# Kernel tuning notes

Measured on AMD Instinct MI355X. Metric: run time of the kernel, lower is better.

Reference implementation:

```python
import jax, jax.numpy as jnp
import numpy as np

N = 50000
E = 800000
IN_C, HID_C, OUT_C = 128, 128, 64


def _glorot(key, shape, gain=1.0):
    fan_in, fan_out = shape[0], shape[1]
    lim = gain * np.sqrt(6.0 / (fan_in + fan_out))
    return jax.random.uniform(key, shape, jnp.float32, -lim, lim)


def setup_inputs() -> dict:
    key = jax.random.key(0)
    ks = jax.random.split(key, 16)
    relu_gain = float(np.sqrt(2.0))
    x = jax.random.normal(ks[0], (N, IN_C), jnp.float32)
    src = jax.random.randint(ks[1], (E,), 0, N, jnp.int64)
    dst = jax.random.randint(ks[2], (E,), 0, N, jnp.int64)
    # layer 0: NGNN_GCNConv(IN_C -> HID_C -> HID_C)
    W0 = _glorot(ks[3], (IN_C, HID_C))
    b0 = jnp.zeros((HID_C,), jnp.float32)
    fcW = _glorot(ks[4], (HID_C, HID_C), relu_gain)
    fcb = jax.random.uniform(ks[5], (HID_C,), jnp.float32, -1, 1) / np.sqrt(HID_C)
    fc2W = _glorot(ks[6], (HID_C, HID_C), relu_gain)
    fc2b = jax.random.uniform(ks[7], (HID_C,), jnp.float32, -1, 1) / np.sqrt(HID_C)
    # layer 1: GraphConv(HID_C -> HID_C)
    W1 = _glorot(ks[8], (HID_C, HID_C))
    b1 = jnp.zeros((HID_C,), jnp.float32)
    # layer 2: GraphConv(HID_C -> OUT_C)
    W2 = _glorot(ks[9], (HID_C, OUT_C))
    b2 = jnp.zeros((OUT_C,), jnp.float32)
    return dict(x=x, src=src, dst=dst, W0=W0, b0=b0, fcW=fcW, fcb=fcb,
                fc2W=fc2W, fc2b=fc2b, W1=W1, b1=b1, W2=W2, b2=b2)


def _degree_norms(src, dst):
    ones = jnp.ones((E,), jnp.float32)
    deg_out = jnp.clip(jax.ops.segment_sum(ones, src, num_segments=N), 1.0)
    deg_in = jnp.clip(jax.ops.segment_sum(ones, dst, num_segments=N), 1.0)
    return jax.lax.rsqrt(deg_out), jax.lax.rsqrt(deg_in)


def _graph_conv(x, W, b, src, dst, nsrc, ndst):
    # DGL GraphConv, norm='both': out = D_in^{-1/2} A (D_out^{-1/2} x W) + b
    h = (x * nsrc[:, None]) @ W            # [N, out_c]
    agg = jax.ops.segment_sum(h[src], dst, num_segments=N)  # gather + scatter-add
    return agg * ndst[:, None] + b


def reference(x, src, dst, W0, b0, fcW, fcb, fc2W, fc2b, W1, b1, W2, b2):
    nsrc, ndst = _degree_norms(src, dst)
    # layer 0: NGNN_GCNConv -> relu (dropout: eval-mode identity)
    h = _graph_conv(x, W0, b0, src, dst, nsrc, ndst)
    h = jax.nn.relu(h)
    h = jax.nn.relu(h @ fcW + fcb)
    h = h @ fc2W + fc2b
    h = jax.nn.relu(h)
    # layer 1: GraphConv -> relu
    h = jax.nn.relu(_graph_conv(h, W1, b1, src, dst, nsrc, ndst))
    # layer 2: GraphConv (no activation)
    return _graph_conv(h, W2, b2, src, dst, nsrc, ndst)
```

## Files before the change

### kernel.cpp

```cpp
#include <hip/hip_runtime.h>
#include <hip/hip_bf16.h>

#define NN 50000
#define NE 800000
#define PAD 56

typedef __attribute__((ext_vector_type(8))) short bf16x8;
typedef __attribute__((ext_vector_type(4))) float f32x4;
typedef __attribute__((ext_vector_type(8))) unsigned short u16x8;

__device__ __forceinline__ unsigned short f2bf(float f) {
    __hip_bfloat16 h = __float2bfloat16(f);
    return *(unsigned short*)&h;
}
__device__ __forceinline__ float bf2f(unsigned short u) {
    unsigned int w = ((unsigned int)u) << 16;
    return __uint_as_float(w);
}

__device__ __forceinline__ void split8(const float* __restrict__ p, bf16x8& h8, bf16x8& l8) {
    float4 v0 = *(const float4*)p;
    float4 v1 = *(const float4*)(p + 4);
    float f[8] = {v0.x, v0.y, v0.z, v0.w, v1.x, v1.y, v1.z, v1.w};
#pragma unroll
    for (int i = 0; i < 8; ++i) {
        unsigned short h = f2bf(f[i]);
        h8[i] = (short)h;
        l8[i] = (short)f2bf(f[i] - bf2f(h));
    }
}

#define DEG_BLK 64
#define DEG_CHUNK 12500
#define DEG_WORDS 12500
#define GEMM0_BLK 782
#define CVW_ELEMS 57344
#define CVW_BLK 224

__global__ __launch_bounds__(256) void hists_kernel(
    const int* __restrict__ src, const int* __restrict__ dst,
    unsigned* __restrict__ psrc, unsigned* __restrict__ pdst,
    const float* __restrict__ x, const float* __restrict__ W0, unsigned short* __restrict__ Hb,
    const float* __restrict__ fcW, const float* __restrict__ fc2W,
    const float* __restrict__ W1, const float* __restrict__ W2,
    unsigned short* __restrict__ wp_hi, unsigned short* __restrict__ wp_lo) {
    __shared__ unsigned hist[DEG_WORDS];
    const int bid = blockIdx.x;
    const int tid = threadIdx.x;
    if (bid < 2 * DEG_BLK) {
        const int dblk = (bid < DEG_BLK) ? bid : bid - DEG_BLK;
        const int* ep = (bid < DEG_BLK) ? src : dst;
        unsigned* outp = ((bid < DEG_BLK) ? psrc : pdst) + (size_t)dblk * DEG_WORDS;
        for (int i = tid; i < DEG_WORDS; i += 256) hist[i] = 0;
        __syncthreads();
        const int4* sp = (const int4*)(ep + dblk * DEG_CHUNK);
        for (int i = tid; i < DEG_CHUNK / 4; i += 256) {
            int4 s = sp[i];
            atomicAdd(&hist[s.x >> 2], 1u << ((s.x & 3) * 8));
            atomicAdd(&hist[s.y >> 2], 1u << ((s.y & 3) * 8));
            atomicAdd(&hist[s.z >> 2], 1u << ((s.z & 3) * 8));
            atomicAdd(&hist[s.w >> 2], 1u << ((s.w & 3) * 8));
        }
        __syncthreads();
        for (int i = tid; i < DEG_WORDS; i += 256) outp[i] = hist[i];
    } else if (bid < 2 * DEG_BLK + CVW_BLK) {
        int t = (bid - 2 * DEG_BLK) * 256 + tid;
        if (t < CVW_ELEMS) {
            int mi = (t < 16384) ? 0 : (t < 32768) ? 1 : (t < 49152) ? 2 : 3;
            int beg = mi * 16384;
            int Cm = (mi == 3) ? 64 : 128;
            int loc = t - beg;
            int k = loc / Cm, c = loc % Cm;
            float v;
            switch (mi) {
                case 0: v = fcW[loc]; break;
                case 1: v = fc2W[loc]; break;
                case 2: v = W1[loc]; break;
                default: v = W2[loc]; break;
            }
            unsigned short h = f2bf(v);
            unsigned short l = f2bf(v - bf2f(h));
            int off = (((c >> 4) * 4 + (k >> 5)) * 64 + ((k & 31) >> 3) * 16 + (c & 15)) * 8 + (k & 7);
            wp_hi[beg + off] = h;
            wp_lo[beg + off] = l;
        }
    } else {
        const int gb = bid - 2 * DEG_BLK - CVW_BLK;
        const int wave = tid >> 6;
        const int lane = tid & 63;
        const int m = lane & 15, kg = lane >> 4;
        const int r0 = gb * 64 + wave * 16;
        int ar = r0 + m;
        ar = (ar < NN) ? ar : (NN - 1);

        bf16x8 ah[4], al[4];
#pragma unroll
        for (int ks = 0; ks < 4; ++ks)
            split8(&x[(size_t)ar * 128 + ks * 32 + kg * 8], ah[ks], al[ks]);

#pragma unroll
        for (int ct = 0; ct < 8; ++ct) {
            f32x4 acc = {0.f, 0.f, 0.f, 0.f};
            const int n = ct * 16 + m;
#pragma unroll
            for (int ks = 0; ks < 4; ++ks) {
                float w[8];
#pragma unroll
                for (int i = 0; i < 8; ++i)
                    w[i] = W0[(size_t)(ks * 32 + kg * 8 + i) * 128 + n];
                bf16x8 bh, bl;
#pragma unroll
                for (int i = 0; i < 8; ++i) {
                    unsigned short h = f2bf(w[i]);
                    bh[i] = (short)h;
                    bl[i] = (short)f2bf(w[i] - bf2f(h));
                }
                acc = __builtin_amdgcn_mfma_f32_16x16x32_bf16(ah[ks], bh, acc, 0, 0, 0);
                acc = __builtin_amdgcn_mfma_f32_16x16x32_bf16(al[ks], bh, acc, 0, 0, 0);
                acc = __builtin_amdgcn_mfma_f32_16x16x32_bf16(ah[ks], bl, acc, 0, 0, 0);
            }
#pragma unroll
            for (int j = 0; j < 4; ++j) {
                const int ra = r0 + 4 * kg + j;
                if (ra < NN) Hb[(size_t)ra * 128 + n] = f2bf(acc[j]);
            }
        }
    }
}

__global__ __launch_bounds__(256) void merge_scan(unsigned* __restrict__ psrc,
                                                  unsigned* __restrict__ pdst,
                                                  int* __restrict__ degout,
                                                  int* __restrict__ cnt) {
    const int idx = blockIdx.x * 256 + threadIdx.x;
    if (idx >= DEG_WORDS) return;
    {
        int a0 = 0, a1 = 0, a2 = 0, a3 = 0;
#pragma unroll 8
        for (int p = 0; p < DEG_BLK; ++p) {
            unsigned w = psrc[(size_t)p * DEG_WORDS + idx];
            a0 += w & 0xFF; a1 += (w >> 8) & 0xFF; a2 += (w >> 16) & 0xFF; a3 += (w >> 24);
        }
        ((int4*)degout)[idx] = make_int4(a0, a1, a2, a3);
    }
    {
        int r0 = 0, r1 = 0, r2 = 0, r3 = 0;
#pragma unroll 8
        for (int p = 0; p < DEG_BLK; ++p) {
            const size_t o = (size_t)p * DEG_WORDS + idx;
            unsigned w = pdst[o];
            pdst[o] = (unsigned)r0 | ((unsigned)r1 << 8) | ((unsigned)r2 << 16) | ((unsigned)r3 << 24);
            r0 += w & 0xFF; r1 += (w >> 8) & 0xFF; r2 += (w >> 16) & 0xFF; r3 += (w >> 24);
        }
        ((int4*)cnt)[idx] = make_int4(r0, r1, r2, r3);
    }
}

__global__ __launch_bounds__(256) void fillc_kernel(const int* __restrict__ src,
                                                    const int* __restrict__ dst,
                                                    const unsigned* __restrict__ pdst,
                                                    unsigned short* __restrict__ col) {
    __shared__ unsigned hist[DEG_WORDS];
    const int dblk = blockIdx.x;
    const int tid = threadIdx.x;
    const unsigned* bp = pdst + (size_t)dblk * DEG_WORDS;
    for (int i = tid; i < DEG_WORDS; i += 256) hist[i] = bp[i];
    __syncthreads();
    const int4* sp = (const int4*)(src + dblk * DEG_CHUNK);
    const int4* dp = (const int4*)(dst + dblk * DEG_CHUNK);
    for (int i = tid; i < DEG_CHUNK / 4; i += 256) {
        int4 s = sp[i];
        int4 d = dp[i];
#pragma unroll
        for (int u = 0; u < 4; ++u) {
            const int dd = (u == 0) ? d.x : (u == 1) ? d.y : (u == 2) ? d.z : d.w;
            const int ss = (u == 0) ? s.x : (u == 1) ? s.y : (u == 2) ? s.z : s.w;
            const unsigned sh = (dd & 3) * 8;
            const unsigned old = atomicAdd(&hist[dd >> 2], 1u << sh);
            const int slot = (old >> sh) & 0xFF;
            col[dd * PAD + slot] = (unsigned short)ss;
        }
    }
}

template <int C>
__global__ __launch_bounds__(256) void mfma_gemm(
    const float* __restrict__ A,
    const unsigned short* __restrict__ Bhi, const unsigned short* __restrict__ Blo,
    const int* __restrict__ degS,
    unsigned short* __restrict__ Yb, int N) {
    constexpr int NT = C / 16;
    const int wave = threadIdx.x >> 6;
    const int lane = threadIdx.x & 63;
    const int m = lane & 15, kg = lane >> 4;
    const int r0 = blockIdx.x * 128 + wave * 32;

    bf16x8 ah0[4], al0[4], ah1[4], al1[4];
#pragma unroll
    for (int t = 0; t < 2; ++t) {
        int ar = r0 + t * 16 + m;
        ar = (ar < N) ? ar : (N - 1);
#pragma unroll
        for (int ks = 0; ks < 4; ++ks) {
            bf16x8 h8, l8;
            split8(&A[(size_t)ar * 128 + ks * 32 + kg * 8], h8, l8);
            if (t == 0) { ah0[ks] = h8; al0[ks] = l8; }
            else        { ah1[ks] = h8; al1[ks] = l8; }
        }
    }

    float sc0[4], sc1[4];
#pragma unroll
    for (int j = 0; j < 4; ++j) {
        int ra = r0 + 4 * kg + j;       ra = (ra < N) ? ra : (N - 1);
        int rb = r0 + 16 + 4 * kg + j;  rb = (rb < N) ? rb : (N - 1);
        int da = degS[ra], db = degS[rb];
        sc0[j] = rsqrtf((float)(da > 1 ? da : 1));
        sc1[j] = rsqrtf((float)(db > 1 ? db : 1));
    }

#pragma unroll
    for (int ct = 0; ct < NT; ++ct) {
        f32x4 acc0 = {0.f, 0.f, 0.f, 0.f};
        f32x4 acc1 = {0.f, 0.f, 0.f, 0.f};
#pragma unroll
        for (int ks = 0; ks < 4; ++ks) {
            const size_t base = ((size_t)(ct * 4 + ks) * 64 + lane) * 8;
            bf16x8 bh = *(const bf16x8*)&Bhi[base];
            bf16x8 bl = *(const bf16x8*)&Blo[base];
            acc0 = __builtin_amdgcn_mfma_f32_16x16x32_bf16(ah0[ks], bh, acc0, 0, 0, 0);
            acc1 = __builtin_amdgcn_mfma_f32_16x16x32_bf16(ah1[ks], bh, acc1, 0, 0, 0);
            acc0 = __builtin_amdgcn_mfma_f32_16x16x32_bf16(al0[ks], bh, acc0, 0, 0, 0);
            acc1 = __builtin_amdgcn_mfma_f32_16x16x32_bf16(al1[ks], bh, acc1, 0, 0, 0);
            acc0 = __builtin_amdgcn_mfma_f32_16x16x32_bf16(ah0[ks], bl, acc0, 0, 0, 0);
            acc1 = __builtin_amdgcn_mfma_f32_16x16x32_bf16(ah1[ks], bl, acc1, 0, 0, 0);
        }
        const int n = ct * 16 + m;
#pragma unroll
        for (int j = 0; j < 4; ++j) {
            const int ra = r0 + 4 * kg + j;
            if (ra < N) Yb[(size_t)ra * C + n] = f2bf(acc0[j] * sc0[j]);
            const int rb = r0 + 16 + 4 * kg + j;
            if (rb < N) Yb[(size_t)rb * C + n] = f2bf(acc1[j] * sc1[j]);
        }
    }
}

__device__ __forceinline__ void t_write(float (*T)[128], int lr, int n, float v) {
    T[lr][((((n >> 2) ^ (lr & 31)) << 2) | (n & 3))] = v;
}
__device__ __forceinline__ void split8_lds(const float (*T)[128], int lr, int c, bf16x8& h8, bf16x8& l8) {
    const int c4 = c >> 2, xr = lr & 31;
    float4 v0 = *(const float4*)&T[lr][(c4 ^ xr) << 2];
    float4 v1 = *(const float4*)&T[lr][((c4 + 1) ^ xr) << 2];
    float f[8] = {v0.x, v0.y, v0.z, v0.w, v1.x, v1.y, v1.z, v1.w};
#pragma unroll
    for (int i = 0; i < 8; ++i) {
        unsigned short h = f2bf(f[i]);
        h8[i] = (short)h;
        l8[i] = (short)f2bf(f[i] - bf2f(h));
    }
}

#define MFMA3(BH, BL) \
    acc = __builtin_amdgcn_mfma_f32_16x16x32_bf16(ah[ks], BH, acc, 0, 0, 0); \
    acc = __builtin_amdgcn_mfma_f32_16x16x32_bf16(al[ks], BH, acc, 0, 0, 0); \
    acc = __builtin_amdgcn_mfma_f32_16x16x32_bf16(ah[ks], BL, acc, 0, 0, 0);

#define LOAD_FRAGS_T() \
    _Pragma("unroll") \
    for (int ks = 0; ks < 4; ++ks) \
        split8_lds(T, wr + m, ks * 32 + kg * 8, ah[ks], al[ks]);

__global__ __launch_bounds__(256) void fused3_kernel(
    const float* __restrict__ A,
    const unsigned short* __restrict__ fwh, const unsigned short* __restrict__ fwl,
    const float* __restrict__ fcb,
    const unsigned short* __restrict__ f2h, const unsigned short* __restrict__ f2l,
    const float* __restrict__ fc2b,
    const unsigned short* __restrict__ w1h, const unsigned short* __restrict__ w1l,
    const int* __restrict__ degS,
    unsigned short* __restrict__ Yb, int N) {
    __shared__ float T[32][128];
    const int wave = threadIdx.x >> 6;
    const int lane = threadIdx.x & 63;
    const int m = lane & 15, kg = lane >> 4;
    const int rowg = wave >> 1;
    const int colh = wave & 1;
    const int r0 = blockIdx.x * 32;
    const int wr = rowg * 16;

    bf16x8 ah[4], al[4];
    {
        int ar = r0 + wr + m;
        ar = (ar < N) ? ar : (N - 1);
#pragma unroll
        for (int ks = 0; ks < 4; ++ks)
            split8(&A[(size_t)ar * 128 + ks * 32 + kg * 8], ah[ks], al[ks]);
    }

#pragma unroll
    for (int ct = 0; ct < 4; ++ct) {
        const int CT = colh * 4 + ct;
        f32x4 acc = {0.f, 0.f, 0.f, 0.f};
#pragma unroll
        for (int ks = 0; ks < 4; ++ks) {
            const size_t base = ((size_t)(CT * 4 + ks) * 64 + lane) * 8;
            bf16x8 bh = *(const bf16x8*)&fwh[base];
            bf16x8 bl = *(const bf16x8*)&fwl[base];
            MFMA3(bh, bl)
        }
        const int n = CT * 16 + m;
        const float bb = fcb[n];
#pragma unroll
        for (int j = 0; j < 4; ++j)
            t_write(T, wr + 4 * kg + j, n, fmaxf(acc[j] + bb, 0.f));
    }
    __syncthreads();
    LOAD_FRAGS_T();
    __syncthreads();

#pragma unroll
    for (int ct = 0; ct < 4; ++ct) {
        const int CT = colh * 4 + ct;
        f32x4 acc = {0.f, 0.f, 0.f, 0.f};
#pragma unroll
        for (int ks = 0; ks < 4; ++ks) {
            const size_t base = ((size_t)(CT * 4 + ks) * 64 + lane) * 8;
            bf16x8 bh = *(const bf16x8*)&f2h[base];
            bf16x8 bl = *(const bf16x8*)&f2l[base];
            MFMA3(bh, bl)
        }
        const int n = CT * 16 + m;
        const float bb = fc2b[n];
#pragma unroll
        for (int j = 0; j < 4; ++j)
            t_write(T, wr + 4 * kg + j, n, fmaxf(acc[j] + bb, 0.f));
    }
    __syncthreads();
    LOAD_FRAGS_T();

#pragma unroll
    for (int ct = 0; ct < 4; ++ct) {
        const int CT = colh * 4 + ct;
        f32x4 acc = {0.f, 0.f, 0.f, 0.f};
#pragma unroll
        for (int ks = 0; ks < 4; ++ks) {
            const size_t base = ((size_t)(CT * 4 + ks) * 64 + lane) * 8;
            bf16x8 bh = *(const bf16x8*)&w1h[base];
            bf16x8 bl = *(const bf16x8*)&w1l[base];
            MFMA3(bh, bl)
        }
        const int n = CT * 16 + m;
#pragma unroll
        for (int j = 0; j < 4; ++j) {
            const int ra = r0 + wr + 4 * kg + j;
            if (ra < N) {
                int dg = degS[ra];
                Yb[(size_t)ra * 128 + n] = f2bf(acc[j] * rsqrtf((float)(dg > 1 ? dg : 1)));
            }
        }
    }
}

template <int C, int RELU, int SCALE_SRC>
__global__ __launch_bounds__(256) void gather_kernel(
    const unsigned short* __restrict__ H, const int* __restrict__ cnt,
    const int* __restrict__ degS, const unsigned short* __restrict__ col,
    const float* __restrict__ bias, float* __restrict__ OUT, int N) {
    constexpr int LPN = C / 8;
    constexpr int NPB = 256 / LPN;
    const int node = blockIdx.x * NPB + threadIdx.x / LPN;
    const int q = threadIdx.x % LPN;
    if (node >= N) return;
    const int deg = cnt[node];
    const unsigned short* cl = col + node * PAD;
    float acc[8];
#pragma unroll
    for (int k = 0; k < 8; ++k) acc[k] = 0.f;
    const int nch = (deg + 7) >> 3;
    for (int ch = 0; ch < nch; ++ch) {
        const int jb = ch * 8;
        u16x8 si = *(const u16x8*)&cl[jb];
        u16x8 hv[8];
        float mm[8];
#pragma unroll
        for (int i = 0; i < 8; ++i) {
            const bool live = (jb + i < deg);
            int s = live ? (int)si[i] : 0;
            hv[i] = *(const u16x8*)&H[(size_t)s * C + q * 8];
            if (SCALE_SRC) {
                int dg = degS[s];
                float r = rsqrtf((float)(dg > 1 ? dg : 1));
                mm[i] = live ? r : 0.f;
            } else {
                mm[i] = live ? 1.f : 0.f;
            }
        }
#pragma unroll
        for (int i = 0; i < 8; ++i) {
#pragma unroll
            for (int k = 0; k < 8; ++k)
                acc[k] = fmaf(bf2f((unsigned short)hv[i][k]), mm[i], acc[k]);
        }
    }
    const float scv = rsqrtf((float)(deg > 1 ? deg : 1));
    const int cb = q * 8;
    float4 o0, o1;
    {
        const float4 b0 = *(const float4*)&bias[cb];
        const float4 b1 = *(const float4*)&bias[cb + 4];
        o0.x = acc[0] * scv + b0.x; o0.y = acc[1] * scv + b0.y;
        o0.z = acc[2] * scv + b0.z; o0.w = acc[3] * scv + b0.w;
        o1.x = acc[4] * scv + b1.x; o1.y = acc[5] * scv + b1.y;
        o1.z = acc[6] * scv + b1.z; o1.w = acc[7] * scv + b1.w;
    }
    if (RELU) {
        o0.x = fmaxf(o0.x, 0.f); o0.y = fmaxf(o0.y, 0.f);
        o0.z = fmaxf(o0.z, 0.f); o0.w = fmaxf(o0.w, 0.f);
        o1.x = fmaxf(o1.x, 0.f); o1.y = fmaxf(o1.y, 0.f);
        o1.z = fmaxf(o1.z, 0.f); o1.w = fmaxf(o1.w, 0.f);
    }
    *(float4*)&OUT[(size_t)node * C + cb] = o0;
    *(float4*)&OUT[(size_t)node * C + cb + 4] = o1;
}

extern "C" void kernel_launch(void* const* d_in, const int* in_sizes, int n_in,
                              void* d_out, int out_size, void* d_ws, size_t ws_size,
                              hipStream_t stream) {
    const float* x    = (const float*)d_in[0];
    const int*   src  = (const int*)d_in[1];
    const int*   dst  = (const int*)d_in[2];
    const float* W0   = (const float*)d_in[3];
    const float* b0   = (const float*)d_in[4];
    const float* fcW  = (const float*)d_in[5];
    const float* fcb  = (const float*)d_in[6];
    const float* fc2W = (const float*)d_in[7];
    const float* fc2b = (const float*)d_in[8];
    const float* W1   = (const float*)d_in[9];
    const float* b1   = (const float*)d_in[10];
    const float* W2   = (const float*)d_in[11];
    const float* b2   = (const float*)d_in[12];
    float* out = (float*)d_out;

    char* ws = (char*)d_ws;
    int* cnt    = (int*)ws;
    int* degout = cnt + NN;
    unsigned short* col = (unsigned short*)(degout + NN);
    unsigned short* wp_hi = col + (size_t)NN * PAD;
    unsigned short* wp_lo = wp_hi + CVW_ELEMS;
    size_t p = ((size_t)(2 * NN) * 4 + (size_t)NN * PAD * 2 + (size_t)CVW_ELEMS * 4 + 255) & ~(size_t)255;
    unsigned* psrc = (unsigned*)(ws + p);
    unsigned* pdst = psrc + (size_t)DEG_BLK * DEG_WORDS;
    size_t p1 = (p + (size_t)2 * DEG_BLK * DEG_WORDS * 4 + 255) & ~(size_t)255;
    unsigned short* Hb = (unsigned short*)(ws + p1);
    size_t p2 = (p1 + (size_t)NN * 128 * 2 + 255) & ~(size_t)255;
    float* bufA = (float*)(ws + p2);

    const unsigned short *fwh = wp_hi,          *fwl = wp_lo;
    const unsigned short *f2h = wp_hi + 16384,  *f2l = wp_lo + 16384;
    const unsigned short *w1h = wp_hi + 32768,  *w1l = wp_lo + 32768;
    const unsigned short *w2h = wp_hi + 49152,  *w2l = wp_lo + 49152;

    hists_kernel<<<2 * DEG_BLK + CVW_BLK + GEMM0_BLK, 256, 0, stream>>>(
        src, dst, psrc, pdst, x, W0, Hb, fcW, fc2W, W1, W2, wp_hi, wp_lo);
    merge_scan<<<(DEG_WORDS + 255) / 256, 256, 0, stream>>>(psrc, pdst, degout, cnt);
    fillc_kernel<<<DEG_BLK, 256, 0, stream>>>(src, dst, pdst, col);

    const int gf = (NN + 31) / 32;
    const int gg = (NN + 127) / 128;
    const int g128 = (NN + 15) / 16;
    const int g64  = (NN + 31) / 32;

    gather_kernel<128, 1, 1><<<g128, 256, 0, stream>>>(Hb, cnt, degout, col, b0, bufA, NN);
    fused3_kernel<<<gf, 256, 0, stream>>>(bufA, fwh, fwl, fcb, f2h, f2l, fc2b, w1h, w1l, degout, Hb, NN);

    gather_kernel<128, 1, 0><<<g128, 256, 0, stream>>>(Hb, cnt, nullptr, col, b1, bufA, NN);

    mfma_gemm<64><<<gg, 256, 0, stream>>>(bufA, w2h, w2l, degout, Hb, NN);
    gather_kernel<64, 0, 0><<<g64, 256, 0, stream>>>(Hb, cnt, nullptr, col, b2, out, NN);
}
```

Measured before the change: 175.1 us.

## Fuse neighbor gathers into following GEMM kernels and split dst histogram finer

Measured after the change: 161.2 us. -7.9%, faster.

```diff
diff --git a/kernel.cpp b/kernel.cpp
--- a/kernel.cpp
+++ b/kernel.cpp
@@ -30,8 +30,10 @@
     }
 }
 
-#define DEG_BLK 64
-#define DEG_CHUNK 12500
+#define SRC_BLK 64
+#define SRC_CHUNK 12500
+#define DST_BLK 160
+#define DST_CHUNK 5000
 #define DEG_WORDS 12500
 #define GEMM0_BLK 782
 #define CVW_ELEMS 57344
@@ -47,14 +49,16 @@
     __shared__ unsigned hist[DEG_WORDS];
     const int bid = blockIdx.x;
     const int tid = threadIdx.x;
-    if (bid < 2 * DEG_BLK) {
-        const int dblk = (bid < DEG_BLK) ? bid : bid - DEG_BLK;
-        const int* ep = (bid < DEG_BLK) ? src : dst;
-        unsigned* outp = ((bid < DEG_BLK) ? psrc : pdst) + (size_t)dblk * DEG_WORDS;
+    if (bid < SRC_BLK + DST_BLK) {
+        const bool isSrc = bid < SRC_BLK;
+        const int dblk = isSrc ? bid : bid - SRC_BLK;
+        const int chunk = isSrc ? SRC_CHUNK : DST_CHUNK;
+        const int* ep = isSrc ? (src + dblk * SRC_CHUNK) : (dst + dblk * DST_CHUNK);
+        unsigned* outp = (isSrc ? psrc : pdst) + (size_t)dblk * DEG_WORDS;
         for (int i = tid; i < DEG_WORDS; i += 256) hist[i] = 0;
         __syncthreads();
-        const int4* sp = (const int4*)(ep + dblk * DEG_CHUNK);
-        for (int i = tid; i < DEG_CHUNK / 4; i += 256) {
+        const int4* sp = (const int4*)ep;
+        for (int i = tid; i < chunk / 4; i += 256) {
             int4 s = sp[i];
             atomicAdd(&hist[s.x >> 2], 1u << ((s.x & 3) * 8));
             atomicAdd(&hist[s.y >> 2], 1u << ((s.y & 3) * 8));
@@ -63,8 +67,8 @@
         }
         __syncthreads();
         for (int i = tid; i < DEG_WORDS; i += 256) outp[i] = hist[i];
-    } else if (bid < 2 * DEG_BLK + CVW_BLK) {
-        int t = (bid - 2 * DEG_BLK) * 256 + tid;
+    } else if (bid < SRC_BLK + DST_BLK + CVW_BLK) {
+        int t = (bid - SRC_BLK - DST_BLK) * 256 + tid;
         if (t < CVW_ELEMS) {
             int mi = (t < 16384) ? 0 : (t < 32768) ? 1 : (t < 49152) ? 2 : 3;
             int beg = mi * 16384;
@@ -85,7 +89,7 @@
             wp_lo[beg + off] = l;
         }
     } else {
-        const int gb = bid - 2 * DEG_BLK - CVW_BLK;
+        const int gb = bid - SRC_BLK - DST_BLK - CVW_BLK;
         const int wave = tid >> 6;
         const int lane = tid & 63;
         const int m = lane & 15, kg = lane >> 4;
@@ -137,7 +141,7 @@
     {
         int a0 = 0, a1 = 0, a2 = 0, a3 = 0;
 #pragma unroll 8
-        for (int p = 0; p < DEG_BLK; ++p) {
+        for (int p = 0; p < SRC_BLK; ++p) {
             unsigned w = psrc[(size_t)p * DEG_WORDS + idx];
             a0 += w & 0xFF; a1 += (w >> 8) & 0xFF; a2 += (w >> 16) & 0xFF; a3 += (w >> 24);
         }
@@ -146,7 +150,7 @@
     {
         int r0 = 0, r1 = 0, r2 = 0, r3 = 0;
 #pragma unroll 8
-        for (int p = 0; p < DEG_BLK; ++p) {
+        for (int p = 0; p < DST_BLK; ++p) {
             const size_t o = (size_t)p * DEG_WORDS + idx;
             unsigned w = pdst[o];
             pdst[o] = (unsigned)r0 | ((unsigned)r1 << 8) | ((unsigned)r2 << 16) | ((unsigned)r3 << 24);
@@ -166,9 +170,9 @@
     const unsigned* bp = pdst + (size_t)dblk * DEG_WORDS;
     for (int i = tid; i < DEG_WORDS; i += 256) hist[i] = bp[i];
     __syncthreads();
-    const int4* sp = (const int4*)(src + dblk * DEG_CHUNK);
-    const int4* dp = (const int4*)(dst + dblk * DEG_CHUNK);
-    for (int i = tid; i < DEG_CHUNK / 4; i += 256) {
+    const int4* sp = (const int4*)(src + dblk * DST_CHUNK);
+    const int4* dp = (const int4*)(dst + dblk * DST_CHUNK);
+    for (int i = tid; i < DST_CHUNK / 4; i += 256) {
         int4 s = sp[i];
         int4 d = dp[i];
 #pragma unroll
@@ -183,69 +187,9 @@
     }
 }
 
-template <int C>
-__global__ __launch_bounds__(256) void mfma_gemm(
-    const float* __restrict__ A,
-    const unsigned short* __restrict__ Bhi, const unsigned short* __restrict__ Blo,
-    const int* __restrict__ degS,
-    unsigned short* __restrict__ Yb, int N) {
-    constexpr int NT = C / 16;
-    const int wave = threadIdx.x >> 6;
-    const int lane = threadIdx.x & 63;
-    const int m = lane & 15, kg = lane >> 4;
-    const int r0 = blockIdx.x * 128 + wave * 32;
-
-    bf16x8 ah0[4], al0[4], ah1[4], al1[4];
-#pragma unroll
-    for (int t = 0; t < 2; ++t) {
-        int ar = r0 + t * 16 + m;
-        ar = (ar < N) ? ar : (N - 1);
-#pragma unroll
-        for (int ks = 0; ks < 4; ++ks) {
-            bf16x8 h8, l8;
-            split8(&A[(size_t)ar * 128 + ks * 32 + kg * 8], h8, l8);
-            if (t == 0) { ah0[ks] = h8; al0[ks] = l8; }
-            else        { ah1[ks] = h8; al1[ks] = l8; }
-        }
-    }
-
-    float sc0[4], sc1[4];
-#pragma unroll
-    for (int j = 0; j < 4; ++j) {
-        int ra = r0 + 4 * kg + j;       ra = (ra < N) ? ra : (N - 1);
-        int rb = r0 + 16 + 4 * kg + j;  rb = (rb < N) ? rb : (N - 1);
-        int da = degS[ra], db = degS[rb];
-        sc0[j] = rsqrtf((float)(da > 1 ? da : 1));
-        sc1[j] = rsqrtf((float)(db > 1 ? db : 1));
-    }
-
-#pragma unroll
-    for (int ct = 0; ct < NT; ++ct) {
-        f32x4 acc0 = {0.f, 0.f, 0.f, 0.f};
-        f32x4 acc1 = {0.f, 0.f, 0.f, 0.f};
-#pragma unroll
-        for (int ks = 0; ks < 4; ++ks) {
-            const size_t base = ((size_t)(ct * 4 + ks) * 64 + lane) * 8;
-            bf16x8 bh = *(const bf16x8*)&Bhi[base];
-            bf16x8 bl = *(const bf16x8*)&Blo[base];
-            acc0 = __builtin_amdgcn_mfma_f32_16x16x32_bf16(ah0[ks], bh, acc0, 0, 0, 0);
-            acc1 = __builtin_amdgcn_mfma_f32_16x16x32_bf16(ah1[ks], bh, acc1, 0, 0, 0);
-            acc0 = __builtin_amdgcn_mfma_f32_16x16x32_bf16(al0[ks], bh, acc0, 0, 0, 0);
-            acc1 = __builtin_amdgcn_mfma_f32_16x16x32_bf16(al1[ks], bh, acc1, 0, 0, 0);
-            acc0 = __builtin_amdgcn_mfma_f32_16x16x32_bf16(ah0[ks], bl, acc0, 0, 0, 0);
-            acc1 = __builtin_amdgcn_mfma_f32_16x16x32_bf16(ah1[ks], bl, acc1, 0, 0, 0);
-        }
-        const int n = ct * 16 + m;
-#pragma unroll
-        for (int j = 0; j < 4; ++j) {
-            const int ra = r0 + 4 * kg + j;
-            if (ra < N) Yb[(size_t)ra * C + n] = f2bf(acc0[j] * sc0[j]);
-            const int rb = r0 + 16 + 4 * kg + j;
-            if (rb < N) Yb[(size_t)rb * C + n] = f2bf(acc1[j] * sc1[j]);
-        }
-    }
-}
-
+__device__ __forceinline__ void t_write4(float (*T)[128], int lr, int c, float4 v) {
+    *(float4*)&T[lr][(((c >> 2) ^ (lr & 31)) << 2)] = v;
+}
 __device__ __forceinline__ void t_write(float (*T)[128], int lr, int n, float v) {
     T[lr][((((n >> 2) ^ (lr & 31)) << 2) | (n & 3))] = v;
 }
@@ -262,54 +206,114 @@
     }
 }
 
-#define MFMA3(BH, BL) \
-    acc = __builtin_amdgcn_mfma_f32_16x16x32_bf16(ah[ks], BH, acc, 0, 0, 0); \
-    acc = __builtin_amdgcn_mfma_f32_16x16x32_bf16(al[ks], BH, acc, 0, 0, 0); \
-    acc = __builtin_amdgcn_mfma_f32_16x16x32_bf16(ah[ks], BL, acc, 0, 0, 0);
+template <int SCALE_SRC>
+__device__ __forceinline__ void gather32_to_T(
+    float (*T)[128], const unsigned short* __restrict__ H,
+    const int* __restrict__ cnt, const int* __restrict__ degout,
+    const unsigned short* __restrict__ colp, const float* __restrict__ bias,
+    int r0, int N, int tid) {
+    const int nl = tid >> 3;
+    const int q  = tid & 7;
+    int node = r0 + nl;
+    node = (node < N) ? node : (N - 1);
+    const int deg = cnt[node];
+    const unsigned short* cl = colp + node * PAD;
+    f32x4 acc[4];
+#pragma unroll
+    for (int v = 0; v < 4; ++v) acc[v] = (f32x4){0.f, 0.f, 0.f, 0.f};
+    const int nch = (deg + 3) >> 2;
+    for (int ch = 0; ch < nch; ++ch) {
+        const int jb = ch * 4;
+        ushort4 si = *(const ushort4*)&cl[jb];
+        u16x8 h0[4], h1[4];
+        float mm[4];
+#pragma unroll
+        for (int i = 0; i < 4; ++i) {
+            const bool live = (jb + i < deg);
+            const unsigned short sv = (i == 0) ? si.x : (i == 1) ? si.y : (i == 2) ? si.z : si.w;
+            int s = live ? (int)sv : 0;
+            const unsigned short* hp = &H[(size_t)s * 128 + q * 16];
+            h0[i] = *(const u16x8*)hp;
+            h1[i] = *(const u16x8*)(hp + 8);
+            if (SCALE_SRC) {
+                int dg = degout[s];
+                float r = rsqrtf((float)(dg > 1 ? dg : 1));
+                mm[i] = live ? r : 0.f;
+            } else {
+                mm[i] = live ? 1.f : 0.f;
+            }
+        }
+#pragma unroll
+        for (int i = 0; i < 4; ++i) {
+#pragma unroll
+            for (int k = 0; k < 8; ++k) {
+                acc[k >> 2][k & 3] = fmaf(bf2f((unsigned short)h0[i][k]), mm[i], acc[k >> 2][k & 3]);
+                acc[2 + (k >> 2)][k & 3] = fmaf(bf2f((unsigned short)h1[i][k]), mm[i], acc[2 + (k >> 2)][k & 3]);
+            }
+        }
+    }
+    const float scv = rsqrtf((float)(deg > 1 ? deg : 1));
+#pragma unroll
+    for (int v = 0; v < 4; ++v) {
+        const int c = q * 16 + v * 4;
+        const float4 b = *(const float4*)&bias[c];
+        float4 o;
+        o.x = fmaxf(acc[v][0] * scv + b.x, 0.f);
+        o.y = fmaxf(acc[v][1] * scv + b.y, 0.f);
+        o.z = fmaxf(acc[v][2] * scv + b.z, 0.f);
+        o.w = fmaxf(acc[v][3] * scv + b.w, 0.f);
+        t_write4(T, nl, c, o);
+    }
+}
+
+#define TILE(WH, WL) \
+    f32x4 acc = {0.f, 0.f, 0.f, 0.f}; \
+    _Pragma("unroll") \
+    for (int ks = 0; ks < 4; ++ks) { \
+        const size_t base = ((size_t)(CT * 4 + ks) * 64 + lane) * 8; \
+        bf16x8 bh = *(const bf16x8*)&WH[base]; \
+        bf16x8 bl = *(const bf16x8*)&WL[base]; \
+        acc = __builtin_amdgcn_mfma_f32_16x16x32_bf16(ah[ks], bh, acc, 0, 0, 0); \
+        acc = __builtin_amdgcn_mfma_f32_16x16x32_bf16(al[ks], bh, acc, 0, 0, 0); \
+        acc = __builtin_amdgcn_mfma_f32_16x16x32_bf16(ah[ks], bl, acc, 0, 0, 0); \
+    }
 
 #define LOAD_FRAGS_T() \
     _Pragma("unroll") \
     for (int ks = 0; ks < 4; ++ks) \
         split8_lds(T, wr + m, ks * 32 + kg * 8, ah[ks], al[ks]);
 
-__global__ __launch_bounds__(256) void fused3_kernel(
-    const float* __restrict__ A,
+__global__ __launch_bounds__(256) void g0f3_kernel(
+    const unsigned short* __restrict__ H,
+    const int* __restrict__ cnt, const int* __restrict__ degout,
+    const unsigned short* __restrict__ colp, const float* __restrict__ b0,
     const unsigned short* __restrict__ fwh, const unsigned short* __restrict__ fwl,
     const float* __restrict__ fcb,
     const unsigned short* __restrict__ f2h, const unsigned short* __restrict__ f2l,
     const float* __restrict__ fc2b,
     const unsigned short* __restrict__ w1h, const unsigned short* __restrict__ w1l,
-    const int* __restrict__ degS,
     unsigned short* __restrict__ Yb, int N) {
     __shared__ float T[32][128];
-    const int wave = threadIdx.x >> 6;
-    const int lane = threadIdx.x & 63;
+    const int tid = threadIdx.x;
+    const int wave = tid >> 6;
+    const int lane = tid & 63;
     const int m = lane & 15, kg = lane >> 4;
     const int rowg = wave >> 1;
     const int colh = wave & 1;
     const int r0 = blockIdx.x * 32;
     const int wr = rowg * 16;
 
+    gather32_to_T<1>(T, H, cnt, degout, colp, b0, r0, N, tid);
+    __syncthreads();
+
     bf16x8 ah[4], al[4];
-    {
-        int ar = r0 + wr + m;
-        ar = (ar < N) ? ar : (N - 1);
-#pragma unroll
-        for (int ks = 0; ks < 4; ++ks)
-            split8(&A[(size_t)ar * 128 + ks * 32 + kg * 8], ah[ks], al[ks]);
-    }
+    LOAD_FRAGS_T();
+    __syncthreads();
 
 #pragma unroll
     for (int ct = 0; ct < 4; ++ct) {
         const int CT = colh * 4 + ct;
-        f32x4 acc = {0.f, 0.f, 0.f, 0.f};
-#pragma unroll
-        for (int ks = 0; ks < 4; ++ks) {
-            const size_t base = ((size_t)(CT * 4 + ks) * 64 + lane) * 8;
-            bf16x8 bh = *(const bf16x8*)&fwh[base];
-            bf16x8 bl = *(const bf16x8*)&fwl[base];
-            MFMA3(bh, bl)
-        }
+        TILE(fwh, fwl)
         const int n = CT * 16 + m;
         const float bb = fcb[n];
 #pragma unroll
@@ -323,14 +327,7 @@
 #pragma unroll
     for (int ct = 0; ct < 4; ++ct) {
         const int CT = colh * 4 + ct;
-        f32x4 acc = {0.f, 0.f, 0.f, 0.f};
-#pragma unroll
-        for (int ks = 0; ks < 4; ++ks) {
-            const size_t base = ((size_t)(CT * 4 + ks) * 64 + lane) * 8;
-            bf16x8 bh = *(const bf16x8*)&f2h[base];
-            bf16x8 bl = *(const bf16x8*)&f2l[base];
-            MFMA3(bh, bl)
-        }
+        TILE(f2h, f2l)
         const int n = CT * 16 + m;
         const float bb = fc2b[n];
 #pragma unroll
@@ -343,33 +340,62 @@
 #pragma unroll
     for (int ct = 0; ct < 4; ++ct) {
         const int CT = colh * 4 + ct;
-        f32x4 acc = {0.f, 0.f, 0.f, 0.f};
-#pragma unroll
-        for (int ks = 0; ks < 4; ++ks) {
-            const size_t base = ((size_t)(CT * 4 + ks) * 64 + lane) * 8;
-            bf16x8 bh = *(const bf16x8*)&w1h[base];
-            bf16x8 bl = *(const bf16x8*)&w1l[base];
-            MFMA3(bh, bl)
-        }
+        TILE(w1h, w1l)
         const int n = CT * 16 + m;
 #pragma unroll
         for (int j = 0; j < 4; ++j) {
             const int ra = r0 + wr + 4 * kg + j;
             if (ra < N) {
-                int dg = degS[ra];
+                int dg = degout[ra];
                 Yb[(size_t)ra * 128 + n] = f2bf(acc[j] * rsqrtf((float)(dg > 1 ? dg : 1)));
             }
         }
     }
 }
 
-template <int C, int RELU, int SCALE_SRC>
-__global__ __launch_bounds__(256) void gather_kernel(
+__global__ __launch_bounds__(256) void g1g2_kernel(
+    const unsigned short* __restrict__ H,
+    const int* __restrict__ cnt, const int* __restrict__ degout,
+    const unsigned short* __restrict__ colp, const float* __restrict__ b1,
+    const unsigned short* __restrict__ w2h, const unsigned short* __restrict__ w2l,
+    unsigned short* __restrict__ Yb, int N) {
+    __shared__ float T[32][128];
+    const int tid = threadIdx.x;
+    const int wave = tid >> 6;
+    const int lane = tid & 63;
+    const int m = lane & 15, kg = lane >> 4;
+    const int rowg = wave >> 1;
+    const int colh = wave & 1;
+    const int r0 = blockIdx.x * 32;
+    const int wr = rowg * 16;
+
+    gather32_to_T<0>(T, H, cnt, degout, colp, b1, r0, N, tid);
+    __syncthreads();
+
+    bf16x8 ah[4], al[4];
+    LOAD_FRAGS_T();
+
+#pragma unroll
+    for (int ct = 0; ct < 2; ++ct) {
+        const int CT = colh * 2 + ct;
+        TILE(w2h, w2l)
+        const int n = CT * 16 + m;
+#pragma unroll
+        for (int j = 0; j < 4; ++j) {
+            const int ra = r0 + wr + 4 * kg + j;
+            if (ra < N) {
+                int dg = degout[ra];
+                Yb[(size_t)ra * 64 + n] = f2bf(acc[j] * rsqrtf((float)(dg > 1 ? dg : 1)));
+            }
+        }
+    }
+}
+
+__global__ __launch_bounds__(256) void gather2_kernel(
     const unsigned short* __restrict__ H, const int* __restrict__ cnt,
-    const int* __restrict__ degS, const unsigned short* __restrict__ col,
+    const unsigned short* __restrict__ col,
     const float* __restrict__ bias, float* __restrict__ OUT, int N) {
-    constexpr int LPN = C / 8;
-    constexpr int NPB = 256 / LPN;
+    constexpr int C = 64, LPN = 8, NPB = 32;
     const int node = blockIdx.x * NPB + threadIdx.x / LPN;
     const int q = threadIdx.x % LPN;
     if (node >= N) return;
@@ -389,13 +415,7 @@
             const bool live = (jb + i < deg);
             int s = live ? (int)si[i] : 0;
             hv[i] = *(const u16x8*)&H[(size_t)s * C + q * 8];
-            if (SCALE_SRC) {
-                int dg = degS[s];
-                float r = rsqrtf((float)(dg > 1 ? dg : 1));
-                mm[i] = live ? r : 0.f;
-            } else {
-                mm[i] = live ? 1.f : 0.f;
-            }
+            mm[i] = live ? 1.f : 0.f;
         }
 #pragma unroll
         for (int i = 0; i < 8; ++i) {
@@ -407,20 +427,12 @@
     const float scv = rsqrtf((float)(deg > 1 ? deg : 1));
     const int cb = q * 8;
     float4 o0, o1;
-    {
-        const float4 b0 = *(const float4*)&bias[cb];
-        const float4 b1 = *(const float4*)&bias[cb + 4];
-        o0.x = acc[0] * scv + b0.x; o0.y = acc[1] * scv + b0.y;
-        o0.z = acc[2] * scv + b0.z; o0.w = acc[3] * scv + b0.w;
-        o1.x = acc[4] * scv + b1.x; o1.y = acc[5] * scv + b1.y;
-        o1.z = acc[6] * scv + b1.z; o1.w = acc[7] * scv + b1.w;
-    }
-    if (RELU) {
-        o0.x = fmaxf(o0.x, 0.f); o0.y = fmaxf(o0.y, 0.f);
-        o0.z = fmaxf(o0.z, 0.f); o0.w = fmaxf(o0.w, 0.f);
-        o1.x = fmaxf(o1.x, 0.f); o1.y = fmaxf(o1.y, 0.f);
-        o1.z = fmaxf(o1.z, 0.f); o1.w = fmaxf(o1.w, 0.f);
-    }
+    const float4 b0 = *(const float4*)&bias[cb];
+    const float4 b1 = *(const float4*)&bias[cb + 4];
+    o0.x = acc[0] * scv + b0.x; o0.y = acc[1] * scv + b0.y;
+    o0.z = acc[2] * scv + b0.z; o0.w = acc[3] * scv + b0.w;
+    o1.x = acc[4] * scv + b1.x; o1.y = acc[5] * scv + b1.y;
+    o1.z = acc[6] * scv + b1.z; o1.w = acc[7] * scv + b1.w;
     *(float4*)&OUT[(size_t)node * C + cb] = o0;
     *(float4*)&OUT[(size_t)node * C + cb + 4] = o1;
 }
@@ -451,32 +463,25 @@
     unsigned short* wp_lo = wp_hi + CVW_ELEMS;
     size_t p = ((size_t)(2 * NN) * 4 + (size_t)NN * PAD * 2 + (size_t)CVW_ELEMS * 4 + 255) & ~(size_t)255;
     unsigned* psrc = (unsigned*)(ws + p);
-    unsigned* pdst = psrc + (size_t)DEG_BLK * DEG_WORDS;
-    size_t p1 = (p + (size_t)2 * DEG_BLK * DEG_WORDS * 4 + 255) & ~(size_t)255;
-    unsigned short* Hb = (unsigned short*)(ws + p1);
-    size_t p2 = (p1 + (size_t)NN * 128 * 2 + 255) & ~(size_t)255;
-    float* bufA = (float*)(ws + p2);
+    unsigned* pdst = psrc + (size_t)SRC_BLK * DEG_WORDS;
+    size_t p1 = (p + (size_t)(SRC_BLK + DST_BLK) * DEG_WORDS * 4 + 255) & ~(size_t)255;
+    unsigned short* Hb  = (unsigned short*)(ws + p1);
+    unsigned short* Hb2 = Hb + (size_t)NN * 128;
 
     const unsigned short *fwh = wp_hi,          *fwl = wp_lo;
     const unsigned short *f2h = wp_hi + 16384,  *f2l = wp_lo + 16384;
     const unsigned short *w1h = wp_hi + 32768,  *w1l = wp_lo + 32768;
     const unsigned short *w2h = wp_hi + 49152,  *w2l = wp_lo + 49152;
 
-    hists_kernel<<<2 * DEG_BLK + CVW_BLK + GEMM0_BLK, 256, 0, stream>>>(
+    hists_kernel<<<SRC_BLK + DST_BLK + CVW_BLK + GEMM0_BLK, 256, 0, stream>>>(
         src, dst, psrc, pdst, x, W0, Hb, fcW, fc2W, W1, W2, wp_hi, wp_lo);
     merge_scan<<<(DEG_WORDS + 255) / 256, 256, 0, stream>>>(psrc, pdst, degout, cnt);
-    fillc_kernel<<<DEG_BLK, 256, 0, stream>>>(src, dst, pdst, col);
-
-    const int gf = (NN + 31) / 32;
-    const int gg = (NN + 127) / 128;
-    const int g128 = (NN + 15) / 16;
-    const int g64  = (NN + 31) / 32;
-
-    gather_kernel<128, 1, 1><<<g128, 256, 0, stream>>>(Hb, cnt, degout, col, b0, bufA, NN);
-    fused3_kernel<<<gf, 256, 0, stream>>>(bufA, fwh, fwl, fcb, f2h, f2l, fc2b, w1h, w1l, degout, Hb, NN);
-
-    gather_kernel<128, 1, 0><<<g128, 256, 0, stream>>>(Hb, cnt, nullptr, col, b1, bufA, NN);
-
-    mfma_gemm<64><<<gg, 256, 0, stream>>>(bufA, w2h, w2l, degout, Hb, NN);
-    gather_kernel<64, 0, 0><<<g64, 256, 0, stream>>>(Hb, cnt, nullptr, col, b2, out, NN);
-}
+    fillc_kernel<<<DST_BLK, 256, 0, stream>>>(src, dst, pdst, col);
+
+    const int g32 = (NN + 31) / 32;
+
+    g0f3_kernel<<<g32, 256, 0, stream>>>(Hb, cnt, degout, col, b0,
+                                         fwh, fwl, fcb, f2h, f2l, fc2b, w1h, w1l, Hb2, NN);
+    g1g2_kernel<<<g32, 256, 0, stream>>>(Hb2, cnt, degout, col, b1, w2h, w2l, Hb, NN);
+    gather2_kernel<<<g32, 256, 0, stream>>>(Hb, cnt, col, b2, out, NN);
+}
```
